# Optimization experiments

Measured on AMD Instinct MI355X. Metric: run time of the kernel, lower is better.

## Reference

```python
import jax, jax.numpy as jnp
import numpy as np

MARGIN_POS = 1.0
MARGIN_NEG = 0.2
LAMBDA_D = 250.0

B, D, H, W = 2, 128, 64, 64


def setup_inputs() -> dict:
    key = jax.random.key(0)
    k0, k1, k2 = jax.random.split(key, 3)
    descriptors_0 = jax.random.normal(k0, (B, D, H, W), dtype=jnp.float32)
    descriptors_1 = jax.random.normal(k1, (B, D, H, W), dtype=jnp.float32)
    similarity_mask = jax.random.randint(k2, (B, H, W, H, W), 0, 2).astype(jnp.bool_)
    return {
        "descriptors_0": descriptors_0,
        "descriptors_1": descriptors_1,
        "similarity_mask": similarity_mask,
    }


def reference(descriptors_0, descriptors_1, similarity_mask):
    # [B,D,H,W] x [B,D,H,W] -> [B,H,W,H,W] dense pairwise descriptor dot products
    dotprod = jnp.einsum('bdij,bdkl->bijkl', descriptors_0, descriptors_1)
    zero = jnp.zeros((), dtype=dotprod.dtype)
    pos_loss = jnp.maximum(zero, MARGIN_POS - dotprod) * LAMBDA_D
    neg_loss = jnp.maximum(zero, dotprod - MARGIN_NEG)
    return jnp.where(similarity_mask, pos_loss, neg_loss).mean()
```

## Files before the change

### kernel.cpp

```cpp
#include <hip/hip_runtime.h>
#include <hip/hip_bf16.h>
#include <stdint.h>

#define BN 2
#define DN 128
#define MN 4096
#define TOTAL_INV (1.0f / 33554432.0f)
#define NPART 8192

typedef __attribute__((ext_vector_type(8))) short short8;
typedef __attribute__((ext_vector_type(4))) float f32x4;

__device__ static inline unsigned short f2bf(float x) {
  unsigned int u = __float_as_uint(x);
  u += 0x7fffu + ((u >> 16) & 1u);
  return (unsigned short)(u >> 16);
}

__global__ __launch_bounds__(256) void transpose_cvt(
    const float* __restrict__ s0, const float* __restrict__ s1,
    unsigned short* __restrict__ o0, unsigned short* __restrict__ o1) {
  __shared__ float tile[64][65];
  const int tx = threadIdx.x & 63;
  const int ty = threadIdx.x >> 6;
  const int m0 = blockIdx.x * 64;
  const int d0 = blockIdx.y * 64;
  const int b  = blockIdx.z & 1;
  const float* src = (blockIdx.z >> 1) ? s1 : s0;
  unsigned short* dst = (blockIdx.z >> 1) ? o1 : o0;
  src += (size_t)b * DN * MN;
  dst += (size_t)b * MN * DN;
#pragma unroll
  for (int i = 0; i < 16; ++i) {
    int dr = i * 4 + ty;
    tile[dr][tx] = src[(size_t)(d0 + dr) * MN + m0 + tx];
  }
  __syncthreads();
#pragma unroll
  for (int i = 0; i < 16; ++i) {
    int mr = i * 4 + ty;
    dst[(size_t)(m0 + mr) * DN + d0 + tx] = f2bf(tile[tx][mr]);
  }
}

__global__ __launch_bounds__(256, 3) void gemm_loss(
    const unsigned short* __restrict__ A, const unsigned short* __restrict__ Bm,
    const void* __restrict__ maskp, float* __restrict__ part) {
  const int tid  = threadIdx.x;
  const int lane = tid & 63;
  const int wave = tid >> 6;
  const int wm = wave >> 1, wn = wave & 1;
  const int quad = lane >> 4;
  const int l16  = lane & 15;
  const int bz = blockIdx.z;
  const int gm = blockIdx.y * 128 + wm * 64;
  const int gn = blockIdx.x * 128 + wn * 64;

  unsigned sw = ((const unsigned int*)maskp)[lane];
  const bool mask_u8 = (__ballot((sw & 0xFFFFFF00u) != 0u) != 0ull);

  const unsigned short* Ab = A  + (size_t)bz * MN * DN + (size_t)gm * DN;
  const unsigned short* Bb = Bm + (size_t)bz * MN * DN + (size_t)gn * DN;

  f32x4 acc[4][4];
#pragma unroll
  for (int i = 0; i < 4; ++i)
#pragma unroll
    for (int j = 0; j < 4; ++j) acc[i][j] = (f32x4){0.f, 0.f, 0.f, 0.f};

#pragma unroll 1
  for (int kt = 0; kt < 4; ++kt) {
    const int k0 = kt * 32 + quad * 8;
    short8 af[4], bf[4];
#pragma unroll
    for (int mi = 0; mi < 4; ++mi)
      af[mi] = *(const short8*)(Ab + (size_t)(mi * 16 + l16) * DN + k0);
#pragma unroll
    for (int ni = 0; ni < 4; ++ni)
      bf[ni] = *(const short8*)(Bb + (size_t)(ni * 16 + l16) * DN + k0);
#pragma unroll
    for (int mi = 0; mi < 4; ++mi)
#pragma unroll
      for (int ni = 0; ni < 4; ++ni)
        acc[mi][ni] = __builtin_amdgcn_mfma_f32_16x16x32_bf16(
            af[mi], bf[ni], acc[mi][ni], 0, 0, 0);
  }

  const size_t mbase = ((size_t)bz * MN + (size_t)gm) * MN + (size_t)gn;
  const int* mi32 = (const int*)maskp;
  const unsigned char* mu8 = (const unsigned char*)maskp;
  float lsum = 0.0f;
#pragma unroll
  for (int mi = 0; mi < 4; ++mi) {
#pragma unroll
    for (int ni = 0; ni < 4; ++ni) {
      f32x4 v = acc[mi][ni];
#pragma unroll
      for (int r = 0; r < 4; ++r) {
        int m = mi * 16 + quad * 4 + r;
        int n = ni * 16 + l16;
        size_t idx = mbase + (size_t)m * MN + n;
        int msk = mask_u8 ? (int)mu8[idx] : mi32[idx];
        float dot = v[r];
        float pos = fmaxf(0.0f, 1.0f - dot) * 250.0f;
        float neg = fmaxf(0.0f, dot - 0.2f);
        lsum += msk ? pos : neg;
      }
    }
  }
#pragma unroll
  for (int off = 32; off > 0; off >>= 1) lsum += __shfl_xor(lsum, off);
  if (lane == 0) {
    size_t slot =
        (((size_t)bz * gridDim.y + blockIdx.y) * gridDim.x + blockIdx.x) * 4 + wave;
    part[slot] = lsum;
  }
}

__global__ __launch_bounds__(1024) void reduce_partials(
    const float* __restrict__ part, float* __restrict__ out) {
  float s = 0.0f;
#pragma unroll
  for (int i = 0; i < NPART / 1024; ++i) s += part[threadIdx.x + i * 1024];
#pragma unroll
  for (int off = 32; off > 0; off >>= 1) s += __shfl_xor(s, off);
  __shared__ float red[16];
  if ((threadIdx.x & 63) == 0) red[threadIdx.x >> 6] = s;
  __syncthreads();
  if (threadIdx.x == 0) {
    float t = 0.0f;
#pragma unroll
    for (int i = 0; i < 16; ++i) t += red[i];
    *out = t * TOTAL_INV;
  }
}

extern "C" void kernel_launch(void* const* d_in, const int* in_sizes, int n_in,
                              void* d_out, int out_size, void* d_ws, size_t ws_size,
                              hipStream_t stream) {
  const float* d0 = (const float*)d_in[0];
  const float* d1 = (const float*)d_in[1];
  const void* mask = d_in[2];
  float* out = (float*)d_out;

  unsigned short* Aw = (unsigned short*)d_ws;
  unsigned short* Bw = Aw + (size_t)BN * MN * DN;
  float* part = (float*)(Bw + (size_t)BN * MN * DN);

  dim3 g1(MN / 64, DN / 64, BN * 2), b1(256);
  transpose_cvt<<<g1, b1, 0, stream>>>(d0, d1, Aw, Bw);

  dim3 g2(MN / 128, MN / 128, BN), b2(256);
  gemm_loss<<<g2, b2, 0, stream>>>(Aw, Bw, mask, part);

  reduce_partials<<<1, 1024, 0, stream>>>(part, out);
}
```

Measured before the change: 233.9 us.

## Stage A/B tiles in LDS via async global-to-LDS loads in gemm_loss

Each block now cooperatively loads its 128x32 A and B k-slices into shared memory with global_load_lds, then waves read their fragments from LDS. Before, each wave loaded its own fragments straight from global memory, so data shared between waves was fetched more than once. The k-loop is fully unrolled and the occupancy hint in launch_bounds is dropped. In exchange it adds __syncthreads barriers with no double buffering, and the kernel is likely dominated by reading the large mask rather than the GEMM operands.

```diff
diff --git a/kernel.cpp b/kernel.cpp
--- a/kernel.cpp
+++ b/kernel.cpp
@@ -15,6 +15,12 @@
   unsigned int u = __float_as_uint(x);
   u += 0x7fffu + ((u >> 16) & 1u);
   return (unsigned short)(u >> 16);
+}
+
+__device__ static inline void async16(const void* g, void* l) {
+  __builtin_amdgcn_global_load_lds(
+      (const __attribute__((address_space(1))) void*)g,
+      (__attribute__((address_space(3))) void*)l, 16, 0, 0);
 }
 
 __global__ __launch_bounds__(256) void transpose_cvt(
@@ -43,24 +49,25 @@
   }
 }
 
-__global__ __launch_bounds__(256, 3) void gemm_loss(
+__global__ __launch_bounds__(256) void gemm_loss(
     const unsigned short* __restrict__ A, const unsigned short* __restrict__ Bm,
     const void* __restrict__ maskp, float* __restrict__ part) {
+  __shared__ __align__(16) unsigned short As[128 * 32];
+  __shared__ __align__(16) unsigned short Bs[128 * 32];
+
   const int tid  = threadIdx.x;
   const int lane = tid & 63;
   const int wave = tid >> 6;
   const int wm = wave >> 1, wn = wave & 1;
   const int quad = lane >> 4;
   const int l16  = lane & 15;
-  const int bz = blockIdx.z;
-  const int gm = blockIdx.y * 128 + wm * 64;
-  const int gn = blockIdx.x * 128 + wn * 64;
+  const int bn = blockIdx.x, bm = blockIdx.y, bz = blockIdx.z;
 
   unsigned sw = ((const unsigned int*)maskp)[lane];
   const bool mask_u8 = (__ballot((sw & 0xFFFFFF00u) != 0u) != 0ull);
 
-  const unsigned short* Ab = A  + (size_t)bz * MN * DN + (size_t)gm * DN;
-  const unsigned short* Bb = Bm + (size_t)bz * MN * DN + (size_t)gn * DN;
+  const unsigned short* Ab = A  + (size_t)bz * MN * DN + (size_t)(bm * 128) * DN;
+  const unsigned short* Bb = Bm + (size_t)bz * MN * DN + (size_t)(bn * 128) * DN;
 
   f32x4 acc[4][4];
 #pragma unroll
@@ -68,25 +75,37 @@
 #pragma unroll
     for (int j = 0; j < 4; ++j) acc[i][j] = (f32x4){0.f, 0.f, 0.f, 0.f};
 
-#pragma unroll 1
+#pragma unroll
   for (int kt = 0; kt < 4; ++kt) {
-    const int k0 = kt * 32 + quad * 8;
+    const int k0 = kt * 32;
+#pragma unroll
+    for (int p = 0; p < 2; ++p) {
+      int c = tid + p * 256;
+      int row = c >> 2;
+      int cq  = c & 3;
+      async16(Ab + (size_t)row * DN + k0 + cq * 8, As + (size_t)c * 8);
+      async16(Bb + (size_t)row * DN + k0 + cq * 8, Bs + (size_t)c * 8);
+    }
+    __syncthreads();
+
     short8 af[4], bf[4];
 #pragma unroll
     for (int mi = 0; mi < 4; ++mi)
-      af[mi] = *(const short8*)(Ab + (size_t)(mi * 16 + l16) * DN + k0);
+      af[mi] = *(const short8*)(As + (wm * 64 + mi * 16 + l16) * 32 + quad * 8);
 #pragma unroll
     for (int ni = 0; ni < 4; ++ni)
-      bf[ni] = *(const short8*)(Bb + (size_t)(ni * 16 + l16) * DN + k0);
+      bf[ni] = *(const short8*)(Bs + (wn * 64 + ni * 16 + l16) * 32 + quad * 8);
 #pragma unroll
     for (int mi = 0; mi < 4; ++mi)
 #pragma unroll
       for (int ni = 0; ni < 4; ++ni)
         acc[mi][ni] = __builtin_amdgcn_mfma_f32_16x16x32_bf16(
             af[mi], bf[ni], acc[mi][ni], 0, 0, 0);
+    if (kt != 3) __syncthreads();
   }
 
-  const size_t mbase = ((size_t)bz * MN + (size_t)gm) * MN + (size_t)gn;
+  const size_t mbase = ((size_t)bz * MN + (size_t)(bm * 128 + wm * 64)) * MN
+                       + (size_t)(bn * 128 + wn * 64);
   const int* mi32 = (const int*)maskp;
   const unsigned char* mu8 = (const unsigned char*)maskp;
   float lsum = 0.0f;
@@ -112,7 +131,7 @@
   for (int off = 32; off > 0; off >>= 1) lsum += __shfl_xor(lsum, off);
   if (lane == 0) {
     size_t slot =
-        (((size_t)bz * gridDim.y + blockIdx.y) * gridDim.x + blockIdx.x) * 4 + wave;
+        (((size_t)bz * gridDim.y + bm) * gridDim.x + bn) * 4 + wave;
     part[slot] = lsum;
   }
 }
```

After: 209.2 us. 1.12x faster.
